# Performance work log

Measured on AMD Instinct MI355X. Metric: run time of the kernel, lower is better.

## Reference

```python
import jax, jax.numpy as jnp
import numpy as np

BATCH = 4_000_000

def setup_inputs() -> dict:
    key = jax.random.key(0)
    k1, k2, k3 = jax.random.split(key, 3)
    y_pred = jax.random.normal(k1, (BATCH, 6), dtype=jnp.float32)
    # bounds: l_x, u_x, l_y, u_y with l < u guaranteed
    lx = jax.random.uniform(k2, (BATCH,), dtype=jnp.float32, minval=-2.0, maxval=0.0)
    ux = lx + jax.random.uniform(k3, (BATCH,), dtype=jnp.float32, minval=0.1, maxval=2.0)
    ly = lx * 0.5
    uy = ly + (ux - lx)
    constr_para = jnp.stack([lx, ux, ly, uy], axis=1)
    return {"y_pred": y_pred, "constr_para": constr_para}

def reference(y_pred, constr_para):
    # Box QP  min 0.5*(y - y_pred)^2  s.t. l <= y <= u  has closed form clamp.
    # Columns 0..2 (x coords) use [l_x, u_x]; columns 3..5 (y coords) use [l_y, u_y].
    l_x = constr_para[:, 0:1]
    u_x = constr_para[:, 1:2]
    l_y = constr_para[:, 2:3]
    u_y = constr_para[:, 3:4]
    x_part = jnp.clip(y_pred[:, :3], l_x, u_x)
    y_part = jnp.clip(y_pred[:, 3:], l_y, u_y)
    return jnp.concatenate([x_part, y_part], axis=1)
```

## Files before the change

### kernel.cpp

```cpp
#include <hip/hip_runtime.h>


__device__ __forceinline__ float clipf(float x, float lo, float hi) {
    return fminf(fmaxf(x, lo), hi);
}

__global__ void BbProjection_27358941676275_kernel(
        const float* __restrict__ yp,
        const float* __restrict__ cp,
        float* __restrict__ out,
        int npairs) {
    const int stride = gridDim.x * blockDim.x;
    for (int i = blockIdx.x * blockDim.x + threadIdx.x; i < npairs; i += stride) {
        const float4* y4 = reinterpret_cast<const float4*>(yp + (size_t)i * 12);
        float4 a = y4[0];
        float4 b = y4[1];
        float4 c = y4[2];
        const float4* c4 = reinterpret_cast<const float4*>(cp + (size_t)i * 8);
        float4 p0 = c4[0];
        float4 p1 = c4[1];

        float4 o0, o1, o2;
        o0.x = clipf(a.x, p0.x, p0.y);
        o0.y = clipf(a.y, p0.x, p0.y);
        o0.z = clipf(a.z, p0.x, p0.y);
        o0.w = clipf(a.w, p0.z, p0.w);
        o1.x = clipf(b.x, p0.z, p0.w);
        o1.y = clipf(b.y, p0.z, p0.w);
        o1.z = clipf(b.z, p1.x, p1.y);
        o1.w = clipf(b.w, p1.x, p1.y);
        o2.x = clipf(c.x, p1.x, p1.y);
        o2.y = clipf(c.y, p1.z, p1.w);
        o2.z = clipf(c.z, p1.z, p1.w);
        o2.w = clipf(c.w, p1.z, p1.w);

        float4* out4 = reinterpret_cast<float4*>(out + (size_t)i * 12);
        out4[0] = o0;
        out4[1] = o1;
        out4[2] = o2;
    }
}

extern "C" void kernel_launch(void* const* d_in, const int* in_sizes, int n_in,
                              void* d_out, int out_size, void* d_ws, size_t ws_size,
                              hipStream_t stream) {
    const float* yp = (const float*)d_in[0];
    const float* cp = (const float*)d_in[1];
    float* out = (float*)d_out;

    const int batch = in_sizes[0] / 6;
    const int npairs = batch / 2;

    const int block = 256;
    int grid = (npairs + block - 1) / block;
    if (grid > 2048) grid = 2048;
    BbProjection_27358941676275_kernel<<<grid, block, 0, stream>>>(yp, cp, out, npairs);
}
```

Measured before the change: 44.33 us.

## Stage loads and stores through LDS for fully coalesced float4 access

Replaces the grid-stride loop with one pair-group per thread, staged through shared memory. Each block cooperatively loads contiguous float4s so adjacent lanes read adjacent addresses, computes the clamps from LDS, writes results back to LDS, then stores them coalesced with nontemporal stores. The aim is to remove the strided 48-byte-per-thread access pattern and to avoid cache pollution on output. The cost is extra LDS traffic, three barriers, and a much larger grid with no grid-stride loop.

```diff
diff --git a/kernel.cpp b/kernel.cpp
--- a/kernel.cpp
+++ b/kernel.cpp
@@ -1,26 +1,50 @@
 #include <hip/hip_runtime.h>
 
+
+typedef float f4 __attribute__((ext_vector_type(4)));
 
 __device__ __forceinline__ float clipf(float x, float lo, float hi) {
     return fminf(fmaxf(x, lo), hi);
 }
 
-__global__ void BbProjection_27358941676275_kernel(
-        const float* __restrict__ yp,
-        const float* __restrict__ cp,
-        float* __restrict__ out,
+#define TPB 256
+
+__global__ __launch_bounds__(TPB) void BbProjection_27358941676275_kernel(
+        const f4* __restrict__ yp4,
+        const f4* __restrict__ cp4,
+        f4* __restrict__ out4,
         int npairs) {
-    const int stride = gridDim.x * blockDim.x;
-    for (int i = blockIdx.x * blockDim.x + threadIdx.x; i < npairs; i += stride) {
-        const float4* y4 = reinterpret_cast<const float4*>(yp + (size_t)i * 12);
-        float4 a = y4[0];
-        float4 b = y4[1];
-        float4 c = y4[2];
-        const float4* c4 = reinterpret_cast<const float4*>(cp + (size_t)i * 8);
-        float4 p0 = c4[0];
-        float4 p1 = c4[1];
+    __shared__ f4 s_y[TPB * 3];
+    __shared__ f4 s_c[TPB * 2];
 
-        float4 o0, o1, o2;
+    const int t = threadIdx.x;
+    const long long pbase = (long long)blockIdx.x * TPB;
+    const long long ybase = pbase * 3;
+    const long long cbase = pbase * 2;
+    const long long ytot = (long long)npairs * 3;
+    const long long ctot = (long long)npairs * 2;
+
+#pragma unroll
+    for (int r = 0; r < 3; ++r) {
+        long long g = ybase + r * TPB + t;
+        if (g < ytot) s_y[r * TPB + t] = yp4[g];
+    }
+#pragma unroll
+    for (int r = 0; r < 2; ++r) {
+        long long g = cbase + r * TPB + t;
+        if (g < ctot) s_c[r * TPB + t] = cp4[g];
+    }
+    __syncthreads();
+
+    f4 o0, o1, o2;
+    const bool act = (pbase + t) < (long long)npairs;
+    if (act) {
+        f4 a  = s_y[t * 3 + 0];
+        f4 b  = s_y[t * 3 + 1];
+        f4 c  = s_y[t * 3 + 2];
+        f4 p0 = s_c[t * 2 + 0];
+        f4 p1 = s_c[t * 2 + 1];
+
         o0.x = clipf(a.x, p0.x, p0.y);
         o0.y = clipf(a.y, p0.x, p0.y);
         o0.z = clipf(a.z, p0.x, p0.y);
@@ -33,26 +57,32 @@
         o2.y = clipf(c.y, p1.z, p1.w);
         o2.z = clipf(c.z, p1.z, p1.w);
         o2.w = clipf(c.w, p1.z, p1.w);
+    }
+    __syncthreads();
+    if (act) {
+        s_y[t * 3 + 0] = o0;
+        s_y[t * 3 + 1] = o1;
+        s_y[t * 3 + 2] = o2;
+    }
+    __syncthreads();
 
-        float4* out4 = reinterpret_cast<float4*>(out + (size_t)i * 12);
-        out4[0] = o0;
-        out4[1] = o1;
-        out4[2] = o2;
+#pragma unroll
+    for (int r = 0; r < 3; ++r) {
+        long long g = ybase + r * TPB + t;
+        if (g < ytot) __builtin_nontemporal_store(s_y[r * TPB + t], &out4[g]);
     }
 }
 
 extern "C" void kernel_launch(void* const* d_in, const int* in_sizes, int n_in,
                               void* d_out, int out_size, void* d_ws, size_t ws_size,
                               hipStream_t stream) {
-    const float* yp = (const float*)d_in[0];
-    const float* cp = (const float*)d_in[1];
-    float* out = (float*)d_out;
+    const f4* yp4 = (const f4*)d_in[0];
+    const f4* cp4 = (const f4*)d_in[1];
+    f4* out4 = (f4*)d_out;
 
     const int batch = in_sizes[0] / 6;
     const int npairs = batch / 2;
 
-    const int block = 256;
-    int grid = (npairs + block - 1) / block;
-    if (grid > 2048) grid = 2048;
-    BbProjection_27358941676275_kernel<<<grid, block, 0, stream>>>(yp, cp, out, npairs);
+    const int grid = (npairs + TPB - 1) / TPB;
+    BbProjection_27358941676275_kernel<<<grid, TPB, 0, stream>>>(yp4, cp4, out4, npairs);
 }
```

After: 41.91 us. 1.06x faster.
